# Kernel tuning notes

Hardware: AMD Instinct MI355X
Metric: run time of the kernel (lower is better)

Reference implementation:

```python
import jax, jax.numpy as jnp
import numpy as np

HID = 16

def _lrconv(x, edge_index, edge_attr, w1, b1, w2, b2):
    # flow='target_to_source': x_i = x[edge_index[0]], x_j = x[edge_index[1]],
    # aggregate (max) at edge_index[0].
    src = edge_index[0]
    dst = edge_index[1]
    m = jnp.concatenate([x[src], x[dst], edge_attr], axis=-1)  # [E, 2*in+edge]
    m = jax.nn.relu(m @ w1 + b1)
    m = jax.nn.relu(m @ w2 + b2)  # [E, out], all >= 0
    agg = jax.ops.segment_max(m, src, num_segments=x.shape[0])
    # empty segments get -inf in jax; PyG fills with 0. Messages are ReLU'd (>=0),
    # so clamping at 0 is exact.
    return jnp.maximum(agg, 0.0)

def _glorot(key, shape):
    fan_in, fan_out = shape
    lim = float(np.sqrt(6.0 / (fan_in + fan_out)))
    return jax.random.uniform(key, shape, jnp.float32, -lim, lim)

def setup_inputs() -> dict:
    key = jax.random.key(0)
    ks = jax.random.split(key, 16)
    N, E = 100000, 1600000
    x = jax.random.normal(ks[0], (N, 4), jnp.float32)
    edge_index = jax.random.randint(ks[1], (2, E), 0, N, jnp.int64)
    edge_attr = jax.random.normal(ks[2], (E, 8), jnp.float32)
    # conv1: in=4 -> cat dim 4*2+8=16
    c1_w1 = _glorot(ks[3], (16, HID)); c1_b1 = jnp.zeros((HID,), jnp.float32)
    c1_w2 = _glorot(ks[4], (HID, 16)); c1_b2 = jnp.zeros((16,), jnp.float32)
    # conv2: in=16 -> cat dim 16*2+8=40
    c2_w1 = _glorot(ks[5], (40, HID)); c2_b1 = jnp.zeros((HID,), jnp.float32)
    c2_w2 = _glorot(ks[6], (HID, 16)); c2_b2 = jnp.zeros((16,), jnp.float32)
    l1_w = _glorot(ks[7], (16, 16)); l1_b = jnp.zeros((16,), jnp.float32)
    l2_w = _glorot(ks[8], (16, 1)); l2_b = jnp.zeros((1,), jnp.float32)
    return {"x": x, "edge_index": edge_index, "edge_attr": edge_attr,
            "c1_w1": c1_w1, "c1_b1": c1_b1, "c1_w2": c1_w2, "c1_b2": c1_b2,
            "c2_w1": c2_w1, "c2_b1": c2_b1, "c2_w2": c2_w2, "c2_b2": c2_b2,
            "l1_w": l1_w, "l1_b": l1_b, "l2_w": l2_w, "l2_b": l2_b}

def reference(x, edge_index, edge_attr,
              c1_w1, c1_b1, c1_w2, c1_b2,
              c2_w1, c2_b1, c2_w2, c2_b2,
              l1_w, l1_b, l2_w, l2_b):
    h = _lrconv(x, edge_index, edge_attr, c1_w1, c1_b1, c1_w2, c1_b2)   # [N,16]
    h = _lrconv(h, edge_index, edge_attr, c2_w1, c2_b1, c2_w2, c2_b2)   # [N,16]
    h = jax.nn.relu(h @ l1_w + l1_b)
    return h @ l2_w + l2_b  # [N,1]
```

## Files before the change

### kernel.cpp

```cpp
#include <hip/hip_runtime.h>
#include <hip/hip_fp16.h>

#define CHUNK 1024
#define RECB 24

typedef _Float16 half8 __attribute__((ext_vector_type(8)));
typedef _Float16 half4 __attribute__((ext_vector_type(4)));
typedef float floatx4 __attribute__((ext_vector_type(4)));

union H8 { half8 h; unsigned int u[4]; };

__device__ __forceinline__ half8 hmax8(half8 a, half8 b) {
#if __has_builtin(__builtin_elementwise_max)
    return __builtin_elementwise_max(a, b);
#else
    half8 r;
    #pragma unroll
    for (int j = 0; j < 8; ++j) r[j] = a[j] > b[j] ? a[j] : b[j];
    return r;
#endif
}

__device__ __forceinline__ unsigned int pack2f(float a, float b) {
    __half2 h = __floats2half2_rn(a, b);
    return *(unsigned int*)&h;
}

__device__ __forceinline__ half8 load_attr(const char* __restrict__ rec, int et) {
    union { unsigned int u[4]; half8 h; } cv;
    uint2 lo = *(const uint2*)(rec + (size_t)et * RECB + 8);
    uint2 hi = *(const uint2*)(rec + (size_t)et * RECB + 16);
    cv.u[0] = lo.x; cv.u[1] = lo.y; cv.u[2] = hi.x; cv.u[3] = hi.y;
    return cv.h;
}

__global__ __launch_bounds__(256) void rank_cvt(
    const int* __restrict__ ei, const float* __restrict__ x,
    int* __restrict__ deg, unsigned short* __restrict__ r,
    _Float16* __restrict__ xh, int E, int N)
{
    int e = blockIdx.x * 256 + threadIdx.x;
    if (e >= E) return;
    r[e] = (unsigned short)atomicAdd(&deg[ei[e]], 1);
    if (e < N) {
        float4 xv = *(const float4*)(x + (size_t)e * 4);
        half4 hx;
        hx[0] = (_Float16)xv.x; hx[1] = (_Float16)xv.y;
        hx[2] = (_Float16)xv.z; hx[3] = (_Float16)xv.w;
        *(half4*)(xh + (size_t)e * 4) = hx;
    }
}

__global__ __launch_bounds__(256) void scan_chunk_sums(
    const int* __restrict__ v, int* __restrict__ csum, int N)
{
    __shared__ int s[256];
    int base = blockIdx.x * CHUNK;
    int t = threadIdx.x;
    int acc = 0;
    #pragma unroll
    for (int i = 0; i < CHUNK / 256; ++i) {
        int idx = base + t + i * 256;
        if (idx < N) acc += v[idx];
    }
    s[t] = acc; __syncthreads();
    for (int o = 128; o > 0; o >>= 1) {
        if (t < o) s[t] += s[t + o];
        __syncthreads();
    }
    if (t == 0) csum[blockIdx.x] = s[0];
}

__global__ __launch_bounds__(256) void scan_chunk_off(
    const int* __restrict__ csum, int* __restrict__ coff, int nch)
{
    __shared__ int s[256];
    __shared__ int carry;
    int t = threadIdx.x;
    if (t == 0) carry = 0;
    __syncthreads();
    for (int base = 0; base < nch; base += 256) {
        int v = (base + t < nch) ? csum[base + t] : 0;
        s[t] = v; __syncthreads();
        for (int o = 1; o < 256; o <<= 1) {
            int add = (t >= o) ? s[t - o] : 0;
            __syncthreads();
            s[t] += add;
            __syncthreads();
        }
        int excl = carry + (t > 0 ? s[t - 1] : 0);
        if (base + t < nch) coff[base + t] = excl;
        __syncthreads();
        if (t == 0) carry += s[255];
        __syncthreads();
    }
}

__global__ __launch_bounds__(256) void scan_within_excl(
    const int* __restrict__ deg, int* __restrict__ pos,
    const int* __restrict__ coff, int N)
{
    __shared__ int s[256];
    int t = threadIdx.x;
    int base = blockIdx.x * CHUNK + t * 4;
    int v0 = 0, v1 = 0, v2 = 0, v3 = 0;
    if (base + 0 < N) v0 = deg[base + 0];
    if (base + 1 < N) v1 = deg[base + 1];
    if (base + 2 < N) v2 = deg[base + 2];
    if (base + 3 < N) v3 = deg[base + 3];
    s[t] = v0 + v1 + v2 + v3;
    __syncthreads();
    for (int o = 1; o < 256; o <<= 1) {
        int add = (t >= o) ? s[t - o] : 0;
        __syncthreads();
        s[t] += add;
        __syncthreads();
    }
    int run = coff[blockIdx.x] + (t > 0 ? s[t - 1] : 0);
    if (base + 0 < N) pos[base + 0] = run; run += v0;
    if (base + 1 < N) pos[base + 1] = run; run += v1;
    if (base + 2 < N) pos[base + 2] = run; run += v2;
    if (base + 3 < N) pos[base + 3] = run;
}

__global__ __launch_bounds__(256) void scatter_rec(
    const int* __restrict__ ei, const float* __restrict__ ea,
    const int* __restrict__ pos, const unsigned short* __restrict__ r,
    char* __restrict__ rec, int E)
{
    int e = blockIdx.x * 256 + threadIdx.x;
    if (e >= E) return;
    int s = ei[e];
    int d = ei[E + e];
    int p = pos[s] + (int)r[e];
    float4 a0 = *(const float4*)(ea + (size_t)e * 8);
    float4 a1 = *(const float4*)(ea + (size_t)e * 8 + 4);
    unsigned int h0 = pack2f(a0.x, a0.y), h1 = pack2f(a0.z, a0.w);
    unsigned int h2 = pack2f(a1.x, a1.y), h3 = pack2f(a1.z, a1.w);
    char* b = rec + (size_t)p * RECB;
    *(int2*)b         = make_int2(s, d);
    *(uint2*)(b + 8)  = make_uint2(h0, h1);
    *(uint2*)(b + 16) = make_uint2(h2, h3);
}

__global__ __launch_bounds__(256) void edge_mlp1(
    const _Float16* __restrict__ xh,
    const char*  __restrict__ rec,
    const float* __restrict__ w1, const float* __restrict__ b1,
    const float* __restrict__ w2, const float* __restrict__ b2,
    _Float16* __restrict__ m2h,
    int E)
{
    __shared__ _Float16 itm[4][8][16][24];
    int tid = threadIdx.x;
    int w = tid >> 6, lane = tid & 63;
    int e16 = lane & 15, q = lane >> 4;
    int ebase = (blockIdx.x * 4 + w) << 7;
    if (ebase >= E) return;
    int e0 = ebase + lane;
    int e1 = ebase + 64 + lane;

    int s0 = 0, d0 = 0, s1 = 0, d1 = 0;
    if (e0 < E) { int2 p = *(const int2*)(rec + (size_t)e0 * RECB); s0 = p.x; d0 = p.y; }
    if (e1 < E) { int2 p = *(const int2*)(rec + (size_t)e1 * RECB); s1 = p.x; d1 = p.y; }

    half8 B1, B2;
    #pragma unroll
    for (int j = 0; j < 8; ++j) { B1[j] = (_Float16)0.f; B2[j] = (_Float16)0.f; }
    if (q < 2) {
        #pragma unroll
        for (int j = 0; j < 8; ++j) {
            B1[j] = (_Float16)w1[(8 * q + j) * 16 + e16];
            B2[j] = (_Float16)w2[(8 * q + j) * 16 + e16];
        }
    }
    float b1c = b1[e16], b2c = b2[e16];

    half8 A[8];
    #pragma unroll
    for (int t = 0; t < 8; ++t) {
        int tt = t & 3;
        int st = (t < 4) ? __shfl(s0, 16 * tt + e16, 64) : __shfl(s1, 16 * tt + e16, 64);
        int dt = (t < 4) ? __shfl(d0, 16 * tt + e16, 64) : __shfl(d1, 16 * tt + e16, 64);
        half8 a;
        #pragma unroll
        for (int j = 0; j < 8; ++j) a[j] = (_Float16)0.f;
        int et = ebase + 16 * t + e16;
        if (q == 0 && et < E) {
            half4 hs = *(const half4*)(xh + (size_t)st * 4);
            half4 hd = *(const half4*)(xh + (size_t)dt * 4);
            a[0] = hs[0]; a[1] = hs[1]; a[2] = hs[2]; a[3] = hs[3];
            a[4] = hd[0]; a[5] = hd[1]; a[6] = hd[2]; a[7] = hd[3];
        } else if (q == 1 && et < E) {
            a = load_attr(rec, et);
        }
        A[t] = a;
    }

    floatx4 C[8];
    #pragma unroll
    for (int t = 0; t < 8; ++t) {
        floatx4 c = {b1c, b1c, b1c, b1c};
        C[t] = __builtin_amdgcn_mfma_f32_16x16x32_f16(A[t], B1, c, 0, 0, 0);
    }
    #pragma unroll
    for (int t = 0; t < 8; ++t)
        #pragma unroll
        for (int i = 0; i < 4; ++i)
            itm[w][t][4 * q + i][e16] = (_Float16)fmaxf(C[t][i], 0.0f);
    __builtin_amdgcn_wave_barrier();

    half8 A2[8];
    #pragma unroll
    for (int t = 0; t < 8; ++t) {
        half8 a;
        #pragma unroll
        for (int j = 0; j < 8; ++j) a[j] = (_Float16)0.f;
        if (q < 2) a = *(const half8*)&itm[w][t][e16][8 * q];
        A2[t] = a;
    }
    __builtin_amdgcn_wave_barrier();
    floatx4 C2[8];
    #pragma unroll
    for (int t = 0; t < 8; ++t) {
        floatx4 c = {b2c, b2c, b2c, b2c};
        C2[t] = __builtin_amdgcn_mfma_f32_16x16x32_f16(A2[t], B2, c, 0, 0, 0);
    }
    #pragma unroll
    for (int t = 0; t < 8; ++t)
        #pragma unroll
        for (int i = 0; i < 4; ++i)
            itm[w][t][4 * q + i][e16] = (_Float16)C2[t][i];
    __builtin_amdgcn_wave_barrier();

    if (e0 < E) {
        half8 lo = *(const half8*)&itm[w][q][e16][0];
        half8 hi = *(const half8*)&itm[w][q][e16][8];
        *(half8*)(m2h + (size_t)e0 * 16)     = lo;
        *(half8*)(m2h + (size_t)e0 * 16 + 8) = hi;
    }
    if (e1 < E) {
        half8 lo = *(const half8*)&itm[w][q + 4][e16][0];
        half8 hi = *(const half8*)&itm[w][q + 4][e16][8];
        *(half8*)(m2h + (size_t)e1 * 16)     = lo;
        *(half8*)(m2h + (size_t)e1 * 16 + 8) = hi;
    }
}

__global__ __launch_bounds__(256) void edge_mlp2(
    const _Float16* __restrict__ h1,
    const char*  __restrict__ rec,
    const float* __restrict__ w1, const float* __restrict__ b1v,
    const float* __restrict__ w2, const float* __restrict__ b2,
    _Float16* __restrict__ m2h, int E)
{
    __shared__ _Float16 itm[4][8][16][24];
    int tid = threadIdx.x;
    int w = tid >> 6, lane = tid & 63;
    int e16 = lane & 15, q = lane >> 4;
    int ebase = (blockIdx.x * 4 + w) << 7;
    if (ebase >= E) return;
    int e0 = ebase + lane;
    int e1 = ebase + 64 + lane;

    int s0 = 0, d0 = 0, s1 = 0, d1 = 0;
    if (e0 < E) { int2 p = *(const int2*)(rec + (size_t)e0 * RECB); s0 = p.x; d0 = p.y; }
    if (e1 < E) { int2 p = *(const int2*)(rec + (size_t)e1 * RECB); s1 = p.x; d1 = p.y; }

    half8 B1, B2e, BL2;
    #pragma unroll
    for (int j = 0; j < 8; ++j) {
        B1[j] = (_Float16)w1[(8 * q + j) * 16 + e16];
        B2e[j] = (_Float16)0.f; BL2[j] = (_Float16)0.f;
    }
    if (q == 0) {
        #pragma unroll
        for (int j = 0; j < 8; ++j)
            B2e[j] = (_Float16)w1[(32 + j) * 16 + e16];
    }
    if (q < 2) {
        #pragma unroll
        for (int j = 0; j < 8; ++j)
            BL2[j] = (_Float16)w2[(8 * q + j) * 16 + e16];
    }
    float b1c = b1v[e16], b2c = b2[e16];

    half8 A1[8];
    #pragma unroll
    for (int t = 0; t < 8; ++t) {
        int tt = t & 3;
        int st = (t < 4) ? __shfl(s0, 16 * tt + e16, 64) : __shfl(s1, 16 * tt + e16, 64);
        int dt = (t < 4) ? __shfl(d0, 16 * tt + e16, 64) : __shfl(d1, 16 * tt + e16, 64);
        int row = (q < 2) ? st : dt;
        A1[t] = *(const half8*)(h1 + (size_t)row * 16 + 8 * (q & 1));
    }

    floatx4 C[8];
    #pragma unroll
    for (int t = 0; t < 8; ++t) {
        half8 a2;
        #pragma unroll
        for (int j = 0; j < 8; ++j) a2[j] = (_Float16)0.f;
        int et = ebase + 16 * t + e16;
        if (q == 0 && et < E)
            a2 = load_attr(rec, et);
        floatx4 c = {b1c, b1c, b1c, b1c};
        c = __builtin_amdgcn_mfma_f32_16x16x32_f16(a2, B2e, c, 0, 0, 0);
        C[t] = __builtin_amdgcn_mfma_f32_16x16x32_f16(A1[t], B1, c, 0, 0, 0);
    }
    #pragma unroll
    for (int t = 0; t < 8; ++t)
        #pragma unroll
        for (int i = 0; i < 4; ++i)
            itm[w][t][4 * q + i][e16] = (_Float16)fmaxf(C[t][i], 0.0f);
    __builtin_amdgcn_wave_barrier();

    half8 A2L[8];
    #pragma unroll
    for (int t = 0; t < 8; ++t) {
        half8 a;
        #pragma unroll
        for (int j = 0; j < 8; ++j) a[j] = (_Float16)0.f;
        if (q < 2) a = *(const half8*)&itm[w][t][e16][8 * q];
        A2L[t] = a;
    }
    __builtin_amdgcn_wave_barrier();
    floatx4 C2[8];
    #pragma unroll
    for (int t = 0; t < 8; ++t) {
        floatx4 c = {b2c, b2c, b2c, b2c};
        C2[t] = __builtin_amdgcn_mfma_f32_16x16x32_f16(A2L[t], BL2, c, 0, 0, 0);
    }
    #pragma unroll
    for (int t = 0; t < 8; ++t)
        #pragma unroll
        for (int i = 0; i < 4; ++i)
            itm[w][t][4 * q + i][e16] = (_Float16)C2[t][i];
    __builtin_amdgcn_wave_barrier();

    if (e0 < E) {
        half8 lo = *(const half8*)&itm[w][q][e16][0];
        half8 hi = *(const half8*)&itm[w][q][e16][8];
        *(half8*)(m2h + (size_t)e0 * 16)     = lo;
        *(half8*)(m2h + (size_t)e0 * 16 + 8) = hi;
    }
    if (e1 < E) {
        half8 lo = *(const half8*)&itm[w][q + 4][e16][0];
        half8 hi = *(const half8*)&itm[w][q + 4][e16][8];
        *(half8*)(m2h + (size_t)e1 * 16)     = lo;
        *(half8*)(m2h + (size_t)e1 * 16 + 8) = hi;
    }
}

__global__ __launch_bounds__(256) void segmax1_h(
    const _Float16* __restrict__ m2h, const int* __restrict__ pos,
    unsigned int* __restrict__ h1u,
    int N, int E)
{
    int tid = threadIdx.x;
    int n = blockIdx.x * 32 + (tid >> 3);
    if (n >= N) return;
    int g = tid & 7;
    int start = pos[n];
    int end = (n + 1 < N) ? pos[n + 1] : E;

    half8 a0, a1;
    #pragma unroll
    for (int j = 0; j < 8; ++j) { a0[j] = (_Float16)0.f; a1[j] = (_Float16)0.f; }

    for (int k = start + g; k < end; k += 8) {
        half8 v0 = *(const half8*)(m2h + (size_t)k * 16);
        half8 v1 = *(const half8*)(m2h + (size_t)k * 16 + 8);
        a0 = hmax8(a0, v0);
        a1 = hmax8(a1, v1);
    }
    #pragma unroll
    for (int mask = 1; mask < 8; mask <<= 1) {
        H8 x0, x1, y0, y1;
        x0.h = a0; x1.h = a1;
        #pragma unroll
        for (int j = 0; j < 4; ++j) {
            y0.u[j] = __shfl_xor(x0.u[j], mask, 64);
            y1.u[j] = __shfl_xor(x1.u[j], mask, 64);
        }
        a0 = hmax8(a0, y0.h);
        a1 = hmax8(a1, y1.h);
    }
    H8 U0, U1; U0.h = a0; U1.h = a1;
    unsigned int word = (g < 4) ? U0.u[g & 3] : U1.u[g & 3];
    h1u[(size_t)n * 8 + g] = word;
}

__global__ __launch_bounds__(256) void segmax2_head(
    const _Float16* __restrict__ m2h, const int* __restrict__ pos,
    const float* __restrict__ l1w, const float* __restrict__ l1b,
    const float* __restrict__ l2w, const float* __restrict__ l2b,
    float* __restrict__ out, int N, int E)
{
    int tid = threadIdx.x;
    int n = blockIdx.x * 32 + (tid >> 3);
    if (n >= N) return;
    int g = tid & 7;
    int start = pos[n];
    int end = (n + 1 < N) ? pos[n + 1] : E;

    half8 a0, a1;
    #pragma unroll
    for (int j = 0; j < 8; ++j) { a0[j] = (_Float16)0.f; a1[j] = (_Float16)0.f; }

    for (int k = start + g; k < end; k += 8) {
        half8 v0 = *(const half8*)(m2h + (size_t)k * 16);
        half8 v1 = *(const half8*)(m2h + (size_t)k * 16 + 8);
        a0 = hmax8(a0, v0);
        a1 = hmax8(a1, v1);
    }
    #pragma unroll
    for (int mask = 1; mask < 8; mask <<= 1) {
        H8 x0, x1, y0, y1;
        x0.h = a0; x1.h = a1;
        #pragma unroll
        for (int j = 0; j < 4; ++j) {
            y0.u[j] = __shfl_xor(x0.u[j], mask, 64);
            y1.u[j] = __shfl_xor(x1.u[j], mask, 64);
        }
        a0 = hmax8(a0, y0.h);
        a1 = hmax8(a1, y1.h);
    }

    float acc[16];
    #pragma unroll
    for (int j = 0; j < 8; ++j) { acc[j] = (float)a0[j]; acc[8 + j] = (float)a1[j]; }

    float t2[16];
    #pragma unroll
    for (int j = 0; j < 16; ++j) t2[j] = l1b[j];
    #pragma unroll
    for (int kk = 0; kk < 16; ++kk) {
        float ak = acc[kk];
        #pragma unroll
        for (int j = 0; j < 16; ++j) t2[j] = fmaf(ak, l1w[kk * 16 + j], t2[j]);
    }
    float r2 = l2b[0];
    #pragma unroll
    for (int j = 0; j < 16; ++j) r2 = fmaf(fmaxf(t2[j], 0.0f), l2w[j], r2);
    if (g == 0) out[n] = r2;
}

extern "C" void kernel_launch(void* const* d_in, const int* in_sizes, int n_in,
                              void* d_out, int out_size, void* d_ws, size_t ws_size,
                              hipStream_t stream)
{
    const float* x     = (const float*)d_in[0];
    const int*   ei    = (const int*)  d_in[1];
    const float* ea    = (const float*)d_in[2];
    const float* c1_w1 = (const float*)d_in[3];
    const float* c1_b1 = (const float*)d_in[4];
    const float* c1_w2 = (const float*)d_in[5];
    const float* c1_b2 = (const float*)d_in[6];
    const float* c2_w1 = (const float*)d_in[7];
    const float* c2_b1 = (const float*)d_in[8];
    const float* c2_w2 = (const float*)d_in[9];
    const float* c2_b2 = (const float*)d_in[10];
    const float* l1_w  = (const float*)d_in[11];
    const float* l1_b  = (const float*)d_in[12];
    const float* l2_w  = (const float*)d_in[13];
    const float* l2_b  = (const float*)d_in[14];
    float* out = (float*)d_out;

    const int N = in_sizes[0] / 4;
    const int E = in_sizes[2] / 8;
    const int nch = (N + CHUNK - 1) / CHUNK;

    const int BLK = 256;
    const int egrid = (E + BLK - 1) / BLK;
    const int ggrid = (N + 31) / 32;
    const int mgrid = (E + 511) / 512;

    size_t szPos = ((size_t)N * 4 + 15) & ~(size_t)15;
    size_t szR   = ((size_t)E * 2 + 15) & ~(size_t)15;
    size_t szXh  = ((size_t)N * 8 + 15) & ~(size_t)15;
    size_t szH1  = ((size_t)N * 32 + 15) & ~(size_t)15;
    size_t szRec = ((size_t)E * RECB + 15) & ~(size_t)15;
    size_t szM2h = (size_t)E * 32;

    size_t pos_off = 0;
    size_t r_off   = pos_off + szPos;
    size_t xh_off  = r_off   + szR;
    size_t h1_off  = xh_off  + szXh;
    size_t rec_off = h1_off  + szH1;
    size_t m2h_off = rec_off + szRec;
    size_t deg_off = m2h_off;
    size_t cs_off  = deg_off + szPos;
    size_t cf_off  = cs_off + 4096;

    int*            pos  = (int*)  ((char*)d_ws + pos_off);
    unsigned short* r    = (unsigned short*)((char*)d_ws + r_off);
    _Float16*       xh   = (_Float16*)((char*)d_ws + xh_off);
    _Float16*       h1   = (_Float16*)((char*)d_ws + h1_off);
    char*           rec  = (char*) ((char*)d_ws + rec_off);
    _Float16*       m2h  = (_Float16*)((char*)d_ws + m2h_off);
    int*            deg  = (int*)  ((char*)d_ws + deg_off);
    int*            csum = (int*)  ((char*)d_ws + cs_off);
    int*            coff = (int*)  ((char*)d_ws + cf_off);

    hipMemsetAsync(deg, 0, (size_t)N * 4, stream);
    rank_cvt<<<egrid, BLK, 0, stream>>>(ei, x, deg, r, xh, E, N);
    scan_chunk_sums<<<nch, BLK, 0, stream>>>(deg, csum, N);
    scan_chunk_off<<<1, 256, 0, stream>>>(csum, coff, nch);
    scan_within_excl<<<nch, BLK, 0, stream>>>(deg, pos, coff, N);
    scatter_rec<<<egrid, BLK, 0, stream>>>(ei, ea, pos, r, rec, E);
    edge_mlp1<<<mgrid, BLK, 0, stream>>>(xh, rec,
                                         c1_w1, c1_b1, c1_w2, c1_b2, m2h, E);
    segmax1_h<<<ggrid, BLK, 0, stream>>>(m2h, pos, (unsigned int*)h1, N, E);
    edge_mlp2<<<mgrid, BLK, 0, stream>>>(h1, rec,
                                         c2_w1, c2_b1, c2_w2, c2_b2, m2h, E);
    segmax2_head<<<ggrid, BLK, 0, stream>>>(m2h, pos, l1_w, l1_b, l2_w, l2_b,
                                            out, N, E);
}
```

Before: 345.6 us.

## Fuse segment-max into edge MLP kernels via shared-memory atomic max

Drops the per-edge fp16 message buffer and the separate segmented-max kernels. Each edge MLP block now reduces its 512 sorted edges into a shared-memory max table indexed by source node. Interior rows are written directly and boundary rows are merged with global atomicMax on float bits, with a global-atomic fallback when a block spans too many nodes. The intent is to remove the write and re-read of a 16-half-per-edge intermediate. The cost is extra memsets, shared atomics, an fp32 aggregate buffer, a small conversion kernel and a simplified head kernel.

```diff
diff --git a/kernel.cpp b/kernel.cpp
--- a/kernel.cpp
+++ b/kernel.cpp
@@ -3,23 +3,11 @@
 
 #define CHUNK 1024
 #define RECB 24
+#define SPAN 192
 
 typedef _Float16 half8 __attribute__((ext_vector_type(8)));
 typedef _Float16 half4 __attribute__((ext_vector_type(4)));
 typedef float floatx4 __attribute__((ext_vector_type(4)));
-
-union H8 { half8 h; unsigned int u[4]; };
-
-__device__ __forceinline__ half8 hmax8(half8 a, half8 b) {
-#if __has_builtin(__builtin_elementwise_max)
-    return __builtin_elementwise_max(a, b);
-#else
-    half8 r;
-    #pragma unroll
-    for (int j = 0; j < 8; ++j) r[j] = a[j] > b[j] ? a[j] : b[j];
-    return r;
-#endif
-}
 
 __device__ __forceinline__ unsigned int pack2f(float a, float b) {
     __half2 h = __floats2half2_rn(a, b);
@@ -143,22 +131,33 @@
     *(uint2*)(b + 16) = make_uint2(h2, h3);
 }
 
-__global__ __launch_bounds__(256) void edge_mlp1(
+__global__ __launch_bounds__(256) void edge_mlp1_agg(
     const _Float16* __restrict__ xh,
     const char*  __restrict__ rec,
     const float* __restrict__ w1, const float* __restrict__ b1,
     const float* __restrict__ w2, const float* __restrict__ b2,
-    _Float16* __restrict__ m2h,
+    int* __restrict__ aggi,
     int E)
 {
     __shared__ _Float16 itm[4][8][16][24];
+    __shared__ int lmax[SPAN * 16];
     int tid = threadIdx.x;
     int w = tid >> 6, lane = tid & 63;
     int e16 = lane & 15, q = lane >> 4;
-    int ebase = (blockIdx.x * 4 + w) << 7;
-    if (ebase >= E) return;
+    int kb = blockIdx.x * 512;
+    int ebase = kb + (w << 7);
     int e0 = ebase + lane;
     int e1 = ebase + 64 + lane;
+
+    #pragma unroll
+    for (int i = 0; i < SPAN * 16 / 256; ++i) lmax[tid + i * 256] = 0;
+
+    int klast = min(kb + 511, E - 1);
+    int n_first = *(const int*)(rec + (size_t)kb * RECB);
+    int n_last  = *(const int*)(rec + (size_t)klast * RECB);
+    int span = n_last - n_first + 1;
+    bool fb = (span > SPAN);
+    __syncthreads();
 
     int s0 = 0, d0 = 0, s1 = 0, d1 = 0;
     if (e0 < E) { int2 p = *(const int2*)(rec + (size_t)e0 * RECB); s0 = p.x; d0 = p.y; }
@@ -226,42 +225,73 @@
         floatx4 c = {b2c, b2c, b2c, b2c};
         C2[t] = __builtin_amdgcn_mfma_f32_16x16x32_f16(A2[t], B2, c, 0, 0, 0);
     }
-    #pragma unroll
-    for (int t = 0; t < 8; ++t)
-        #pragma unroll
-        for (int i = 0; i < 4; ++i)
-            itm[w][t][4 * q + i][e16] = (_Float16)C2[t][i];
-    __builtin_amdgcn_wave_barrier();
-
-    if (e0 < E) {
-        half8 lo = *(const half8*)&itm[w][q][e16][0];
-        half8 hi = *(const half8*)&itm[w][q][e16][8];
-        *(half8*)(m2h + (size_t)e0 * 16)     = lo;
-        *(half8*)(m2h + (size_t)e0 * 16 + 8) = hi;
-    }
-    if (e1 < E) {
-        half8 lo = *(const half8*)&itm[w][q + 4][e16][0];
-        half8 hi = *(const half8*)&itm[w][q + 4][e16][8];
-        *(half8*)(m2h + (size_t)e1 * 16)     = lo;
-        *(half8*)(m2h + (size_t)e1 * 16 + 8) = hi;
-    }
-}
-
-__global__ __launch_bounds__(256) void edge_mlp2(
+
+    #pragma unroll
+    for (int t = 0; t < 8; ++t) {
+        int tt = t & 3;
+        #pragma unroll
+        for (int i = 0; i < 4; ++i) {
+            int rr = 4 * q + i;
+            int nn = (t < 4) ? __shfl(s0, 16 * tt + rr, 64) : __shfl(s1, 16 * tt + rr, 64);
+            int et = ebase + 16 * t + rr;
+            if (et < E) {
+                int bits = __float_as_int(fmaxf(C2[t][i], 0.0f));
+                if (!fb) atomicMax(&lmax[(nn - n_first) * 16 + e16], bits);
+                else     atomicMax(&aggi[(size_t)nn * 16 + e16], bits);
+            }
+        }
+    }
+    __syncthreads();
+    if (!fb) {
+        int tot = span * 16;
+        for (int idx = tid; idx < tot; idx += 256) {
+            int row = idx >> 4;
+            int nn = n_first + row;
+            int v = lmax[idx];
+            if (nn == n_first || nn == n_last) {
+                if (v != 0) atomicMax(&aggi[(size_t)nn * 16 + (idx & 15)], v);
+            } else {
+                aggi[(size_t)nn * 16 + (idx & 15)] = v;
+            }
+        }
+    }
+}
+
+__global__ __launch_bounds__(256) void cvt_h1(
+    const int* __restrict__ aggi, unsigned int* __restrict__ h1u, int total)
+{
+    int i = blockIdx.x * 256 + threadIdx.x;
+    if (i >= total) return;
+    int2 v = *(const int2*)(aggi + 2 * i);
+    h1u[i] = pack2f(__int_as_float(v.x), __int_as_float(v.y));
+}
+
+__global__ __launch_bounds__(256) void edge_mlp2_agg(
     const _Float16* __restrict__ h1,
     const char*  __restrict__ rec,
     const float* __restrict__ w1, const float* __restrict__ b1v,
     const float* __restrict__ w2, const float* __restrict__ b2,
-    _Float16* __restrict__ m2h, int E)
+    int* __restrict__ aggi, int E)
 {
     __shared__ _Float16 itm[4][8][16][24];
+    __shared__ int lmax[SPAN * 16];
     int tid = threadIdx.x;
     int w = tid >> 6, lane = tid & 63;
     int e16 = lane & 15, q = lane >> 4;
-    int ebase = (blockIdx.x * 4 + w) << 7;
-    if (ebase >= E) return;
+    int kb = blockIdx.x * 512;
+    int ebase = kb + (w << 7);
     int e0 = ebase + lane;
     int e1 = ebase + 64 + lane;
+
+    #pragma unroll
+    for (int i = 0; i < SPAN * 16 / 256; ++i) lmax[tid + i * 256] = 0;
+
+    int klast = min(kb + 511, E - 1);
+    int n_first = *(const int*)(rec + (size_t)kb * RECB);
+    int n_last  = *(const int*)(rec + (size_t)klast * RECB);
+    int span = n_last - n_first + 1;
+    bool fb = (span > SPAN);
+    __syncthreads();
 
     int s0 = 0, d0 = 0, s1 = 0, d1 = 0;
     if (e0 < E) { int2 p = *(const int2*)(rec + (size_t)e0 * RECB); s0 = p.x; d0 = p.y; }
@@ -331,119 +361,63 @@
         floatx4 c = {b2c, b2c, b2c, b2c};
         C2[t] = __builtin_amdgcn_mfma_f32_16x16x32_f16(A2L[t], BL2, c, 0, 0, 0);
     }
-    #pragma unroll
-    for (int t = 0; t < 8; ++t)
-        #pragma unroll
-        for (int i = 0; i < 4; ++i)
-            itm[w][t][4 * q + i][e16] = (_Float16)C2[t][i];
-    __builtin_amdgcn_wave_barrier();
-
-    if (e0 < E) {
-        half8 lo = *(const half8*)&itm[w][q][e16][0];
-        half8 hi = *(const half8*)&itm[w][q][e16][8];
-        *(half8*)(m2h + (size_t)e0 * 16)     = lo;
-        *(half8*)(m2h + (size_t)e0 * 16 + 8) = hi;
-    }
-    if (e1 < E) {
-        half8 lo = *(const half8*)&itm[w][q + 4][e16][0];
-        half8 hi = *(const half8*)&itm[w][q + 4][e16][8];
-        *(half8*)(m2h + (size_t)e1 * 16)     = lo;
-        *(half8*)(m2h + (size_t)e1 * 16 + 8) = hi;
-    }
-}
-
-__global__ __launch_bounds__(256) void segmax1_h(
-    const _Float16* __restrict__ m2h, const int* __restrict__ pos,
-    unsigned int* __restrict__ h1u,
-    int N, int E)
-{
-    int tid = threadIdx.x;
-    int n = blockIdx.x * 32 + (tid >> 3);
-    if (n >= N) return;
-    int g = tid & 7;
-    int start = pos[n];
-    int end = (n + 1 < N) ? pos[n + 1] : E;
-
-    half8 a0, a1;
-    #pragma unroll
-    for (int j = 0; j < 8; ++j) { a0[j] = (_Float16)0.f; a1[j] = (_Float16)0.f; }
-
-    for (int k = start + g; k < end; k += 8) {
-        half8 v0 = *(const half8*)(m2h + (size_t)k * 16);
-        half8 v1 = *(const half8*)(m2h + (size_t)k * 16 + 8);
-        a0 = hmax8(a0, v0);
-        a1 = hmax8(a1, v1);
-    }
-    #pragma unroll
-    for (int mask = 1; mask < 8; mask <<= 1) {
-        H8 x0, x1, y0, y1;
-        x0.h = a0; x1.h = a1;
-        #pragma unroll
-        for (int j = 0; j < 4; ++j) {
-            y0.u[j] = __shfl_xor(x0.u[j], mask, 64);
-            y1.u[j] = __shfl_xor(x1.u[j], mask, 64);
-        }
-        a0 = hmax8(a0, y0.h);
-        a1 = hmax8(a1, y1.h);
-    }
-    H8 U0, U1; U0.h = a0; U1.h = a1;
-    unsigned int word = (g < 4) ? U0.u[g & 3] : U1.u[g & 3];
-    h1u[(size_t)n * 8 + g] = word;
-}
-
-__global__ __launch_bounds__(256) void segmax2_head(
-    const _Float16* __restrict__ m2h, const int* __restrict__ pos,
+
+    #pragma unroll
+    for (int t = 0; t < 8; ++t) {
+        int tt = t & 3;
+        #pragma unroll
+        for (int i = 0; i < 4; ++i) {
+            int rr = 4 * q + i;
+            int nn = (t < 4) ? __shfl(s0, 16 * tt + rr, 64) : __shfl(s1, 16 * tt + rr, 64);
+            int et = ebase + 16 * t + rr;
+            if (et < E) {
+                int bits = __float_as_int(fmaxf(C2[t][i], 0.0f));
+                if (!fb) atomicMax(&lmax[(nn - n_first) * 16 + e16], bits);
+                else     atomicMax(&aggi[(size_t)nn * 16 + e16], bits);
+            }
+        }
+    }
+    __syncthreads();
+    if (!fb) {
+        int tot = span * 16;
+        for (int idx = tid; idx < tot; idx += 256) {
+            int row = idx >> 4;
+            int nn = n_first + row;
+            int v = lmax[idx];
+            if (nn == n_first || nn == n_last) {
+                if (v != 0) atomicMax(&aggi[(size_t)nn * 16 + (idx & 15)], v);
+            } else {
+                aggi[(size_t)nn * 16 + (idx & 15)] = v;
+            }
+        }
+    }
+}
+
+__global__ __launch_bounds__(256) void head_out(
+    const int* __restrict__ aggi,
     const float* __restrict__ l1w, const float* __restrict__ l1b,
     const float* __restrict__ l2w, const float* __restrict__ l2b,
-    float* __restrict__ out, int N, int E)
-{
-    int tid = threadIdx.x;
-    int n = blockIdx.x * 32 + (tid >> 3);
+    float* __restrict__ out, int N)
+{
+    int n = blockIdx.x * 256 + threadIdx.x;
     if (n >= N) return;
-    int g = tid & 7;
-    int start = pos[n];
-    int end = (n + 1 < N) ? pos[n + 1] : E;
-
-    half8 a0, a1;
-    #pragma unroll
-    for (int j = 0; j < 8; ++j) { a0[j] = (_Float16)0.f; a1[j] = (_Float16)0.f; }
-
-    for (int k = start + g; k < end; k += 8) {
-        half8 v0 = *(const half8*)(m2h + (size_t)k * 16);
-        half8 v1 = *(const half8*)(m2h + (size_t)k * 16 + 8);
-        a0 = hmax8(a0, v0);
-        a1 = hmax8(a1, v1);
-    }
-    #pragma unroll
-    for (int mask = 1; mask < 8; mask <<= 1) {
-        H8 x0, x1, y0, y1;
-        x0.h = a0; x1.h = a1;
-        #pragma unroll
-        for (int j = 0; j < 4; ++j) {
-            y0.u[j] = __shfl_xor(x0.u[j], mask, 64);
-            y1.u[j] = __shfl_xor(x1.u[j], mask, 64);
-        }
-        a0 = hmax8(a0, y0.h);
-        a1 = hmax8(a1, y1.h);
-    }
-
-    float acc[16];
-    #pragma unroll
-    for (int j = 0; j < 8; ++j) { acc[j] = (float)a0[j]; acc[8 + j] = (float)a1[j]; }
-
+    const float4* ar = (const float4*)(aggi + (size_t)n * 16);
+    float4 A0 = ar[0], A1 = ar[1], A2 = ar[2], A3 = ar[3];
+    float acc[16] = {A0.x, A0.y, A0.z, A0.w, A1.x, A1.y, A1.z, A1.w,
+                     A2.x, A2.y, A2.z, A2.w, A3.x, A3.y, A3.z, A3.w};
     float t2[16];
     #pragma unroll
     for (int j = 0; j < 16; ++j) t2[j] = l1b[j];
     #pragma unroll
-    for (int kk = 0; kk < 16; ++kk) {
-        float ak = acc[kk];
-        #pragma unroll
-        for (int j = 0; j < 16; ++j) t2[j] = fmaf(ak, l1w[kk * 16 + j], t2[j]);
+    for (int k = 0; k < 16; ++k) {
+        float ak = acc[k];
+        #pragma unroll
+        for (int j = 0; j < 16; ++j) t2[j] = fmaf(ak, l1w[k * 16 + j], t2[j]);
     }
     float r2 = l2b[0];
     #pragma unroll
     for (int j = 0; j < 16; ++j) r2 = fmaf(fmaxf(t2[j], 0.0f), l2w[j], r2);
-    if (g == 0) out[n] = r2;
+    out[n] = r2;
 }
 
 extern "C" void kernel_launch(void* const* d_in, const int* in_sizes, int n_in,
@@ -473,47 +447,54 @@
 
     const int BLK = 256;
     const int egrid = (E + BLK - 1) / BLK;
-    const int ggrid = (N + 31) / 32;
     const int mgrid = (E + 511) / 512;
-
-    size_t szPos = ((size_t)N * 4 + 15) & ~(size_t)15;
-    size_t szR   = ((size_t)E * 2 + 15) & ~(size_t)15;
-    size_t szXh  = ((size_t)N * 8 + 15) & ~(size_t)15;
-    size_t szH1  = ((size_t)N * 32 + 15) & ~(size_t)15;
-    size_t szRec = ((size_t)E * RECB + 15) & ~(size_t)15;
-    size_t szM2h = (size_t)E * 32;
-
-    size_t pos_off = 0;
-    size_t r_off   = pos_off + szPos;
-    size_t xh_off  = r_off   + szR;
-    size_t h1_off  = xh_off  + szXh;
-    size_t rec_off = h1_off  + szH1;
-    size_t m2h_off = rec_off + szRec;
-    size_t deg_off = m2h_off;
-    size_t cs_off  = deg_off + szPos;
-    size_t cf_off  = cs_off + 4096;
+    const int ngrid = (N + 255) / 256;
+    const int cgrid = (N * 8 + 255) / 256;
+
+    size_t szPos = ((size_t)N * 4 + 255) & ~(size_t)255;
+    size_t szR   = ((size_t)E * 2 + 255) & ~(size_t)255;
+    size_t szXh  = ((size_t)N * 8 + 255) & ~(size_t)255;
+    size_t szH1  = ((size_t)N * 32 + 255) & ~(size_t)255;
+    size_t szRec = ((size_t)E * RECB + 255) & ~(size_t)255;
+    size_t szAgg = ((size_t)N * 16 * 4 + 255) & ~(size_t)255;
+    size_t szDeg = szPos;
+
+    size_t pos_off  = 0;
+    size_t r_off    = pos_off  + szPos;
+    size_t xh_off   = r_off    + szR;
+    size_t h1_off   = xh_off   + szXh;
+    size_t rec_off  = h1_off   + szH1;
+    size_t agg1_off = rec_off  + szRec;
+    size_t agg2_off = agg1_off + szAgg;
+    size_t deg_off  = agg2_off + szAgg;
+    size_t cs_off   = deg_off  + szDeg;
+    size_t cf_off   = cs_off   + 4096;
 
     int*            pos  = (int*)  ((char*)d_ws + pos_off);
     unsigned short* r    = (unsigned short*)((char*)d_ws + r_off);
     _Float16*       xh   = (_Float16*)((char*)d_ws + xh_off);
     _Float16*       h1   = (_Float16*)((char*)d_ws + h1_off);
     char*           rec  = (char*) ((char*)d_ws + rec_off);
-    _Float16*       m2h  = (_Float16*)((char*)d_ws + m2h_off);
+    int*            agg1 = (int*)  ((char*)d_ws + agg1_off);
+    int*            agg2 = (int*)  ((char*)d_ws + agg2_off);
     int*            deg  = (int*)  ((char*)d_ws + deg_off);
     int*            csum = (int*)  ((char*)d_ws + cs_off);
     int*            coff = (int*)  ((char*)d_ws + cf_off);
 
     hipMemsetAsync(deg, 0, (size_t)N * 4, stream);
+    hipMemsetAsync(agg1, 0, (size_t)N * 64, stream);
+    hipMemsetAsync(agg2, 0, (size_t)N * 64, stream);
     rank_cvt<<<egrid, BLK, 0, stream>>>(ei, x, deg, r, xh, E, N);
     scan_chunk_sums<<<nch, BLK, 0, stream>>>(deg, csum, N);
     scan_chunk_off<<<1, 256, 0, stream>>>(csum, coff, nch);
     scan_within_excl<<<nch, BLK, 0, stream>>>(deg, pos, coff, N);
     scatter_rec<<<egrid, BLK, 0, stream>>>(ei, ea, pos, r, rec, E);
-    edge_mlp1<<<mgrid, BLK, 0, stream>>>(xh, rec,
-                                         c1_w1, c1_b1, c1_w2, c1_b2, m2h, E);
-    segmax1_h<<<ggrid, BLK, 0, stream>>>(m2h, pos, (unsigned int*)h1, N, E);
-    edge_mlp2<<<mgrid, BLK, 0, stream>>>(h1, rec,
-                                         c2_w1, c2_b1, c2_w2, c2_b2, m2h, E);
-    segmax2_head<<<ggrid, BLK, 0, stream>>>(m2h, pos, l1_w, l1_b, l2_w, l2_b,
-                                            out, N, E);
-}
+    edge_mlp1_agg<<<mgrid, BLK, 0, stream>>>(xh, rec,
+                                             c1_w1, c1_b1, c1_w2, c1_b2,
+                                             agg1, E);
+    cvt_h1<<<cgrid, BLK, 0, stream>>>(agg1, (unsigned int*)h1, N * 8);
+    edge_mlp2_agg<<<mgrid, BLK, 0, stream>>>(h1, rec,
+                                             c2_w1, c2_b1, c2_w2, c2_b2,
+                                             agg2, E);
+    head_out<<<ngrid, BLK, 0, stream>>>(agg2, l1_w, l1_b, l2_w, l2_b, out, N);
+}
```

New measurement: 324.9 us. 1.06x faster.
